# Kernel optimization log

Measured on AMD Instinct MI355X. Metric: run time of the kernel, lower is better.

The kernel has to match this reference:

```python
import jax, jax.numpy as jnp
import numpy as np

B, T, C, H = 2, 2048, 1024, 16
HD = C // H
MAX_WAVELENGTH = 10000.0


def apply_rope(x, positions):
    # x: [B, H, T, HD], positions: [T]
    fraction = 2.0 * jnp.arange(HD // 2, dtype=jnp.float32) / HD
    timescale = MAX_WAVELENGTH ** fraction  # [HD//2]
    sinusoid = positions[:, None] / timescale[None, :]  # [T, HD//2]
    sin = jnp.sin(sinusoid)
    cos = jnp.cos(sinusoid)
    first, second = jnp.split(x, 2, axis=-1)
    out = jnp.concatenate(
        [first * cos - second * sin, second * cos + first * sin], axis=-1
    )
    return out.astype(x.dtype)


def setup_inputs() -> dict:
    key = jax.random.key(0)
    k1, k2, k3 = jax.random.split(key, 3)
    x = jax.random.normal(k1, (B, T, C), dtype=jnp.float32)
    w_attn = jax.random.normal(k2, (C, 3 * C), dtype=jnp.float32) * 0.02
    b_attn = jnp.zeros((3 * C,), dtype=jnp.float32)
    w_proj = jax.random.normal(k3, (C, C), dtype=jnp.float32) * 0.02
    b_proj = jnp.zeros((C,), dtype=jnp.float32)
    return {"x": x, "w_attn": w_attn, "b_attn": b_attn,
            "w_proj": w_proj, "b_proj": b_proj}


def reference(x, w_attn, b_attn, w_proj, b_proj):
    b, t, c = x.shape
    qkv = x @ w_attn + b_attn  # [B, T, 3C]
    q, k, v = jnp.split(qkv, 3, axis=-1)
    q = q.reshape(b, t, H, HD).transpose(0, 2, 1, 3)  # [B, H, T, HD]
    k = k.reshape(b, t, H, HD).transpose(0, 2, 1, 3)
    v = v.reshape(b, t, H, HD).transpose(0, 2, 1, 3)
    positions = jnp.arange(t, dtype=x.dtype)
    q = apply_rope(q, positions)
    k = apply_rope(k, positions)
    att = jnp.einsum('bhqd,bhkd->bhqk', q, k) * (1.0 / jnp.sqrt(HD))
    causal = jnp.tril(jnp.ones((t, t), dtype=bool))
    att = jnp.where(causal, att, jnp.finfo(att.dtype).min)
    att = jax.nn.softmax(att, axis=-1)
    y = jnp.einsum('bhqk,bhkd->bhqd', att, v)
    y = y.transpose(0, 2, 1, 3).reshape(b, t, c)
    return y @ w_proj + b_proj
```

## Files before the change

kernel.cpp:

```cpp
#include <hip/hip_runtime.h>
#include <hip/hip_bf16.h>


typedef __attribute__((ext_vector_type(8))) short short8;
typedef __attribute__((ext_vector_type(4))) float floatx4;

__device__ __forceinline__ unsigned short f2bf(float f) {
    union { float f; unsigned int u; } v; v.f = f;
    unsigned int r = v.u + 0x7FFFu + ((v.u >> 16) & 1u);
    return (unsigned short)(r >> 16);
}

__device__ __forceinline__ unsigned int pk2bf(float a, float b) {
    union { float f; unsigned int u; } ua, ub;
    ua.f = a; ub.f = b;
    return __builtin_amdgcn_perm(ub.u + 0x8000u, ua.u + 0x8000u, 0x07060302u);
}

__device__ __forceinline__ void gld16(const void* g, void* l) {
    __builtin_amdgcn_global_load_lds(
        (const __attribute__((address_space(1))) unsigned int*)g,
        (__attribute__((address_space(3))) unsigned int*)l, 16, 0, 0);
}

__device__ __forceinline__ void transpose_body(
    const float* __restrict__ in, unsigned short* __restrict__ out,
    int R, int NC, int bx, int by, int tid,
    unsigned short (*tile)[65]) {
    int r0 = by * 64, c0 = bx * 64;
    int col = tid & 63, rr = tid >> 6;
#pragma unroll
    for (int i = 0; i < 16; i++) {
        int row = rr + i * 4;
        tile[row][col] = f2bf(in[(size_t)(r0 + row) * NC + c0 + col]);
    }
    __syncthreads();
#pragma unroll
    for (int i = 0; i < 16; i++) {
        int orow = rr + i * 4;
        out[(size_t)(c0 + orow) * R + r0 + col] = tile[col][orow];
    }
}

__global__ __launch_bounds__(256) void prep(
    const float* __restrict__ x,
    const float* __restrict__ w_attn,
    const float* __restrict__ w_proj,
    unsigned short* __restrict__ x_bf,
    unsigned short* __restrict__ wTa,
    unsigned short* __restrict__ wTp,
    float2* __restrict__ tab) {
    __shared__ unsigned short tile[64][65];
    int bid = blockIdx.x;
    int tid = threadIdx.x;
    if (bid < 4096) {
        int i = bid * 256 + tid;
        float4 v = ((const float4*)x)[i];
        ushort4 o;
        o.x = f2bf(v.x); o.y = f2bf(v.y); o.z = f2bf(v.z); o.w = f2bf(v.w);
        ((ushort4*)x_bf)[i] = o;
    } else if (bid < 4864) {
        int t = bid - 4096;
        transpose_body(w_attn, wTa, 1024, 3072, t % 48, t / 48, tid, tile);
    } else if (bid < 5120) {
        int t = bid - 4864;
        transpose_body(w_proj, wTp, 1024, 1024, t & 15, t >> 4, tid, tile);
    } else {
        int i = (bid - 5120) * 256 + tid;
        int t = i >> 5, d = i & 31;
        float inv_ts = exp2f(-0.41524101186092036f * (float)d);
        float ang = (float)t * inv_ts;
        tab[i] = make_float2(sinf(ang), cosf(ang));
    }
}

__global__ __launch_bounds__(256) void gemm_qkv(
    const unsigned short* __restrict__ A,
    const unsigned short* __restrict__ BT,
    const float* __restrict__ bias,
    const float2* __restrict__ tab,
    unsigned short* __restrict__ qT,
    unsigned short* __restrict__ kT,
    unsigned short* __restrict__ vT) {
    __shared__ __align__(16) unsigned short smem[16384];
    unsigned short* as = smem;
    unsigned short* bs = smem + 8192;
    int tid = threadIdx.x;
    int lane = tid & 63;
    int w = tid >> 6;
    int wx = w & 1, wy = w >> 1;
    int l16 = lane & 15, quad = lane >> 4;
    int m0 = blockIdx.y * 128;
    int n0 = blockIdx.x * 128;
    int x = l16 & 7;
    int lr = lane >> 3;
    int gc = (lane & 7) ^ lr;

    floatx4 acc[4][4];
#pragma unroll
    for (int mi = 0; mi < 4; mi++)
#pragma unroll
        for (int ni = 0; ni < 4; ni++)
            acc[mi][ni] = (floatx4){0.f, 0.f, 0.f, 0.f};

    for (int k0 = 0; k0 < 1024; k0 += 64) {
        __syncthreads();
#pragma unroll
        for (int i = 0; i < 4; i++) {
            int seg = w * 4 + i;
            int row = seg * 8 + lr;
            gld16(A + (size_t)(m0 + row) * 1024 + k0 + gc * 8, &as[seg * 512]);
            gld16(BT + (size_t)(n0 + row) * 1024 + k0 + gc * 8, &bs[seg * 512]);
        }
        __syncthreads();
#pragma unroll
        for (int kk = 0; kk < 2; kk++) {
            short8 af[4], bf[4];
#pragma unroll
            for (int mi = 0; mi < 4; mi++) {
                int r = wy * 64 + mi * 16 + l16;
                af[mi] = *(const short8*)&as[r * 64 + (((kk << 2) | quad) ^ x) * 8];
            }
#pragma unroll
            for (int ni = 0; ni < 4; ni++) {
                int r = wx * 64 + ni * 16 + l16;
                bf[ni] = *(const short8*)&bs[r * 64 + (((kk << 2) | quad) ^ x) * 8];
            }
#pragma unroll
            for (int mi = 0; mi < 4; mi++)
#pragma unroll
                for (int ni = 0; ni < 4; ni++)
                    acc[mi][ni] = __builtin_amdgcn_mfma_f32_16x16x32_bf16(
                        af[mi], bf[ni], acc[mi][ni], 0, 0, 0);
        }
    }

    int region = n0 >> 10;
    int b = m0 >> 11;
    float b0 = bias[n0 + wx * 64 + l16];
    float b1 = bias[n0 + wx * 64 + 16 + l16];
    float b2 = bias[n0 + wx * 64 + 32 + l16];
    float b3 = bias[n0 + wx * 64 + 48 + l16];

    if (region < 2) {
        unsigned short* qk = region ? kT : qT;
        float scale = region ? 1.0f : 0.125f;
        int h = ((n0 & 1023) + wx * 64) >> 6;
        unsigned short* obase = qk + (size_t)(b * 16 + h) * 2048 * 64;
#pragma unroll
        for (int mi = 0; mi < 4; mi++)
#pragma unroll
            for (int r = 0; r < 4; r++) {
                int t = (m0 & 2047) + wy * 64 + mi * 16 + quad * 4 + r;
                float2 sc0 = tab[t * 32 + l16];
                float2 sc1 = tab[t * 32 + 16 + l16];
                float v1 = acc[mi][0][r] + b0, v2 = acc[mi][2][r] + b2;
                float w1 = acc[mi][1][r] + b1, w2 = acc[mi][3][r] + b3;
                unsigned short* orow = obase + (size_t)t * 64;
                orow[l16]      = f2bf((v1 * sc0.y - v2 * sc0.x) * scale);
                orow[l16 + 32] = f2bf((v2 * sc0.y + v1 * sc0.x) * scale);
                orow[l16 + 16] = f2bf((w1 * sc1.y - w2 * sc1.x) * scale);
                orow[l16 + 48] = f2bf((w2 * sc1.y + w1 * sc1.x) * scale);
            }
    } else {
        __syncthreads();
#pragma unroll
        for (int mi = 0; mi < 4; mi++)
#pragma unroll
            for (int ni = 0; ni < 4; ni++) {
                int d_loc = wx * 64 + ni * 16 + l16;
                int t_base = wy * 64 + mi * 16 + quad * 4;
                float bv = (ni == 0) ? b0 : (ni == 1) ? b1 : (ni == 2) ? b2 : b3;
                uint2 pk;
                pk.x = pk2bf(acc[mi][ni][0] + bv, acc[mi][ni][1] + bv);
                pk.y = pk2bf(acc[mi][ni][2] + bv, acc[mi][ni][3] + bv);
                int e = d_loc * 128 + (t_base ^ ((d_loc & 15) << 3));
                *(uint2*)&smem[e] = pk;
            }
        __syncthreads();
        int d_r = tid >> 1, half = tid & 1;
        int cv = (n0 - 2048) + d_r;
        int hh = cv >> 6, dd = cv & 63;
        int fofs = (d_r & 15) << 3;
        size_t vbase = ((size_t)(b * 16 + hh) * 64 + dd) * 2048 + (m0 & 2047);
#pragma unroll
        for (int c = 0; c < 8; c++) {
            int tc = half * 64 + c * 8;
            short8 val = *(const short8*)&smem[d_r * 128 + (tc ^ fofs)];
            *(short8*)&vT[vbase + tc] = val;
        }
    }
}

__global__ __launch_bounds__(256) void gemm_proj(
    const unsigned short* __restrict__ A,
    const unsigned short* __restrict__ BT,
    const float* __restrict__ bias,
    float* __restrict__ out) {
    __shared__ __align__(16) unsigned short as[128 * 64];
    __shared__ __align__(16) unsigned short bs[64 * 64];
    int lane = threadIdx.x & 63;
    int w = threadIdx.x >> 6;
    int wx = w & 1, wy = w >> 1;
    int l16 = lane & 15, quad = lane >> 4;
    int m0 = blockIdx.y * 128;
    int n0 = blockIdx.x * 64;
    int x = l16 & 7;
    int lr = lane >> 3;
    int gc = (lane & 7) ^ lr;

    floatx4 acc[4][2];
#pragma unroll
    for (int mi = 0; mi < 4; mi++)
#pragma unroll
        for (int ni = 0; ni < 2; ni++)
            acc[mi][ni] = (floatx4){0.f, 0.f, 0.f, 0.f};

    for (int k0 = 0; k0 < 1024; k0 += 64) {
        __syncthreads();
#pragma unroll
        for (int i = 0; i < 6; i++) {
            int seg = w * 6 + i;
            if (seg < 16) {
                int row = seg * 8 + lr;
                gld16(A + (size_t)(m0 + row) * 1024 + k0 + gc * 8, &as[seg * 512]);
            } else {
                int s2 = seg - 16;
                int row = s2 * 8 + lr;
                gld16(BT + (size_t)(n0 + row) * 1024 + k0 + gc * 8, &bs[s2 * 512]);
            }
        }
        __syncthreads();
#pragma unroll
        for (int kk = 0; kk < 2; kk++) {
            short8 af[4], bf[2];
#pragma unroll
            for (int mi = 0; mi < 4; mi++) {
                int r = wy * 64 + mi * 16 + l16;
                af[mi] = *(const short8*)&as[r * 64 + (((kk << 2) | quad) ^ x) * 8];
            }
#pragma unroll
            for (int ni = 0; ni < 2; ni++) {
                int r = wx * 32 + ni * 16 + l16;
                bf[ni] = *(const short8*)&bs[r * 64 + (((kk << 2) | quad) ^ x) * 8];
            }
#pragma unroll
            for (int mi = 0; mi < 4; mi++)
#pragma unroll
                for (int ni = 0; ni < 2; ni++)
                    acc[mi][ni] = __builtin_amdgcn_mfma_f32_16x16x32_bf16(
                        af[mi], bf[ni], acc[mi][ni], 0, 0, 0);
        }
    }

#pragma unroll
    for (int mi = 0; mi < 4; mi++)
#pragma unroll
        for (int ni = 0; ni < 2; ni++) {
            int row = m0 + wy * 64 + mi * 16 + quad * 4;
            int col = n0 + wx * 32 + ni * 16 + l16;
            float bv = bias[col];
#pragma unroll
            for (int r = 0; r < 4; r++)
                out[(size_t)(row + r) * 1024 + col] = acc[mi][ni][r] + bv;
        }
}

__global__ __launch_bounds__(512) void attn4(
    const unsigned short* __restrict__ qT,
    const unsigned short* __restrict__ kT,
    const unsigned short* __restrict__ vT,
    unsigned short* __restrict__ y) {
    __shared__ __align__(16) unsigned short kbuf[2][64 * 64];
    __shared__ __align__(16) unsigned short vbuf[2][64 * 64];
    __shared__ __align__(16) unsigned short pl[8][16 * 88];
    int lane = threadIdx.x & 63;
    int w = threadIdx.x >> 6;
    int l16 = lane & 15, quad = lane >> 4;
    int blk = blockIdx.x;
    int idx = blk >> 5;
    int qb = (idx < 8) ? (15 - idx * 2) : ((idx - 8) * 2);
    int bh = blk & 31;
    int b = bh >> 4, h = bh & 15;
    int q0 = qb * 128 + w * 16;
    int dt = 2 * qb + (w >> 2);
    const unsigned short* qp = qT + (size_t)bh * 2048 * 64;
    const unsigned short* kp = kT + (size_t)bh * 2048 * 64;
    const unsigned short* vp = vT + (size_t)bh * 64 * 2048;
    unsigned short* plw = pl[w];
    int x = l16 & 7;

    short8 qf0 = *(const short8*)(qp + (size_t)(q0 + l16) * 64 + quad * 8);
    short8 qf1 = *(const short8*)(qp + (size_t)(q0 + l16) * 64 + 32 + quad * 8);

    floatx4 acc[4];
#pragma unroll
    for (int ni = 0; ni < 4; ni++) acc[ni] = (floatx4){0.f, 0.f, 0.f, 0.f};
    float l_part = 0.f;

    auto stage = [&](int bi, int j0) {
#pragma unroll
        for (int i = 0; i < 2; i++) {
            int t = w * 2 + i;
            if (t < 8) {
                int r = t * 8 + (lane >> 3);
                int c = (lane & 7) ^ (r & 7);
                gld16(kp + (size_t)(j0 + r) * 64 + c * 8, &kbuf[bi][t * 512]);
            } else {
                int s = t - 8;
                int d = s * 8 + (lane >> 3);
                int c = (lane & 7) ^ (d & 7);
                gld16(vp + (size_t)d * 2048 + j0 + c * 8, &vbuf[bi][s * 512]);
            }
        }
    };

    int L = 2 * qb + 2;
    stage(0, 0);
    for (int it = 0; it < L; it++) {
        int j0 = it * 64;
        int bi = it & 1;
        __syncthreads();
        if (it + 1 < L) stage(bi ^ 1, j0 + 64);
        if (it > dt) continue;
        const unsigned short* kb = kbuf[bi];
        const unsigned short* vb = vbuf[bi];
        bool diag = (it == dt);
        floatx4 s[4];
#pragma unroll
        for (int c = 0; c < 4; c++) {
            int r = c * 16 + l16;
            short8 kf0 = *(const short8*)&kb[r * 64 + ((quad) ^ x) * 8];
            short8 kf1 = *(const short8*)&kb[r * 64 + ((quad | 4) ^ x) * 8];
            floatx4 z = (floatx4){0.f, 0.f, 0.f, 0.f};
            z = __builtin_amdgcn_mfma_f32_16x16x32_bf16(kf0, qf0, z, 0, 0, 0);
            z = __builtin_amdgcn_mfma_f32_16x16x32_bf16(kf1, qf1, z, 0, 0, 0);
            s[c] = z;
        }
        int query = q0 + l16;
#pragma unroll
        for (int c = 0; c < 4; c++) {
            float p[4];
#pragma unroll
            for (int r = 0; r < 4; r++) {
                float e = __expf(s[c][r]);
                if (diag) {
                    int key = j0 + c * 16 + quad * 4 + r;
                    e = (key <= query) ? e : 0.f;
                }
                p[r] = e;
            }
            l_part += (p[0] + p[1]) + (p[2] + p[3]);
            uint2 pk = {pk2bf(p[0], p[1]), pk2bf(p[2], p[3])};
            *(uint2*)&plw[l16 * 88 + c * 16 + quad * 4] = pk;
        }
        short8 pa0 = *(const short8*)&plw[l16 * 88 + quad * 8];
        short8 pa1 = *(const short8*)&plw[l16 * 88 + 32 + quad * 8];
#pragma unroll
        for (int ni = 0; ni < 4; ni++) {
            int d = ni * 16 + l16;
            short8 vf0 = *(const short8*)&vb[d * 64 + ((quad) ^ x) * 8];
            short8 vf1 = *(const short8*)&vb[d * 64 + ((quad | 4) ^ x) * 8];
            acc[ni] = __builtin_amdgcn_mfma_f32_16x16x32_bf16(pa0, vf0, acc[ni], 0, 0, 0);
            acc[ni] = __builtin_amdgcn_mfma_f32_16x16x32_bf16(pa1, vf1, acc[ni], 0, 0, 0);
        }
    }

    float tot = l_part;
    tot += __shfl_xor(tot, 16, 64);
    tot += __shfl_xor(tot, 32, 64);
    float inv[4];
#pragma unroll
    for (int r = 0; r < 4; r++)
        inv[r] = 1.f / __shfl(tot, quad * 4 + r, 16);
#pragma unroll
    for (int ni = 0; ni < 4; ni++)
#pragma unroll
        for (int r = 0; r < 4; r++) {
            int t = q0 + quad * 4 + r;
            y[((size_t)(b * 2048 + t)) * 1024 + h * 64 + ni * 16 + l16] =
                f2bf(acc[ni][r] * inv[r]);
        }
}

extern "C" void kernel_launch(void* const* d_in, const int* in_sizes, int n_in,
                              void* d_out, int out_size, void* d_ws, size_t ws_size,
                              hipStream_t stream) {
    const float* x      = (const float*)d_in[0];
    const float* w_attn = (const float*)d_in[1];
    const float* b_attn = (const float*)d_in[2];
    const float* w_proj = (const float*)d_in[3];
    const float* b_proj = (const float*)d_in[4];
    float* out = (float*)d_out;

    char* ws = (char*)d_ws;
    unsigned short* x_bf = (unsigned short*)ws;
    unsigned short* wTa  = (unsigned short*)(ws + (8ull << 20));
    unsigned short* wTp  = (unsigned short*)(ws + (14ull << 20));
    unsigned short* qTb  = (unsigned short*)(ws + (16ull << 20));
    unsigned short* kTb  = (unsigned short*)(ws + (24ull << 20));
    unsigned short* vTb  = (unsigned short*)(ws + (32ull << 20));
    float2*         tab  = (float2*)(ws + (40ull << 20));
    unsigned short* y_bf = x_bf;

    prep<<<5376, 256, 0, stream>>>(x, w_attn, w_proj, x_bf, wTa, wTp, tab);
    gemm_qkv<<<dim3(24, 32), 256, 0, stream>>>(x_bf, wTa, b_attn, tab,
                                               qTb, kTb, vTb);
    attn4<<<512, 512, 0, stream>>>(qTb, kTb, vTb, y_bf);
    gemm_proj<<<dim3(16, 32), 256, 0, stream>>>(y_bf, wTp, b_proj, out);
}
```

Baseline: 186.8 us.

## Double-buffer LDS tiles in QKV and proj GEMMs and coalesce Q/K stores

Both GEMM kernels now use two LDS buffers, so the async global-to-LDS load of the next K tile is issued before computing on the current tile, removing one barrier per iteration and overlapping loads with MFMA work. The QKV epilogue for Q/K regions first writes the rope-rotated bf16 results into padded LDS rows and then stores full 16-byte vectors per row instead of scattered 2-byte stores. This doubles LDS usage per block (64KB for qkv), which may reduce occupancy.

```diff
diff --git a/kernel.cpp b/kernel.cpp
--- a/kernel.cpp
+++ b/kernel.cpp
@@ -82,9 +82,7 @@
     unsigned short* __restrict__ qT,
     unsigned short* __restrict__ kT,
     unsigned short* __restrict__ vT) {
-    __shared__ __align__(16) unsigned short smem[16384];
-    unsigned short* as = smem;
-    unsigned short* bs = smem + 8192;
+    __shared__ __align__(16) unsigned short smem[32768];
     int tid = threadIdx.x;
     int lane = tid & 63;
     int w = tid >> 6;
@@ -103,8 +101,9 @@
         for (int ni = 0; ni < 4; ni++)
             acc[mi][ni] = (floatx4){0.f, 0.f, 0.f, 0.f};
 
-    for (int k0 = 0; k0 < 1024; k0 += 64) {
-        __syncthreads();
+    auto stage = [&](int bsel, int k0) {
+        unsigned short* as = smem + bsel * 16384;
+        unsigned short* bs = as + 8192;
 #pragma unroll
         for (int i = 0; i < 4; i++) {
             int seg = w * 4 + i;
@@ -112,7 +111,11 @@
             gld16(A + (size_t)(m0 + row) * 1024 + k0 + gc * 8, &as[seg * 512]);
             gld16(BT + (size_t)(n0 + row) * 1024 + k0 + gc * 8, &bs[seg * 512]);
         }
-        __syncthreads();
+    };
+
+    auto compute = [&](int bsel) {
+        const unsigned short* as = smem + bsel * 16384;
+        const unsigned short* bs = as + 8192;
 #pragma unroll
         for (int kk = 0; kk < 2; kk++) {
             short8 af[4], bf[4];
@@ -133,7 +136,19 @@
                     acc[mi][ni] = __builtin_amdgcn_mfma_f32_16x16x32_bf16(
                         af[mi], bf[ni], acc[mi][ni], 0, 0, 0);
         }
-    }
+    };
+
+    stage(0, 0);
+    __syncthreads();
+    int cur = 0;
+    for (int k0 = 0; k0 < 960; k0 += 64) {
+        stage(cur ^ 1, k0 + 64);
+        compute(cur);
+        __syncthreads();
+        cur ^= 1;
+    }
+    compute(cur);
+    __syncthreads();
 
     int region = n0 >> 10;
     int b = m0 >> 11;
@@ -145,25 +160,37 @@
     if (region < 2) {
         unsigned short* qk = region ? kT : qT;
         float scale = region ? 1.0f : 0.125f;
-        int h = ((n0 & 1023) + wx * 64) >> 6;
-        unsigned short* obase = qk + (size_t)(b * 16 + h) * 2048 * 64;
+        unsigned short* lq = smem;
 #pragma unroll
         for (int mi = 0; mi < 4; mi++)
 #pragma unroll
             for (int r = 0; r < 4; r++) {
-                int t = (m0 & 2047) + wy * 64 + mi * 16 + quad * 4 + r;
+                int tl = wy * 64 + mi * 16 + quad * 4 + r;
+                int t = (m0 & 2047) + tl;
                 float2 sc0 = tab[t * 32 + l16];
                 float2 sc1 = tab[t * 32 + 16 + l16];
                 float v1 = acc[mi][0][r] + b0, v2 = acc[mi][2][r] + b2;
                 float w1 = acc[mi][1][r] + b1, w2 = acc[mi][3][r] + b3;
-                unsigned short* orow = obase + (size_t)t * 64;
+                unsigned short* orow = lq + tl * 136 + wx * 64;
                 orow[l16]      = f2bf((v1 * sc0.y - v2 * sc0.x) * scale);
                 orow[l16 + 32] = f2bf((v2 * sc0.y + v1 * sc0.x) * scale);
                 orow[l16 + 16] = f2bf((w1 * sc1.y - w2 * sc1.x) * scale);
                 orow[l16 + 48] = f2bf((w2 * sc1.y + w1 * sc1.x) * scale);
             }
+        __syncthreads();
+        int c8 = tid & 7;
+        int hl = (tid >> 3) & 1;
+        int tl0 = tid >> 4;
+        int h = ((n0 & 1023) >> 6) + hl;
+        unsigned short* ob = qk + (size_t)(b * 16 + h) * 2048 * 64;
+#pragma unroll
+        for (int p = 0; p < 8; p++) {
+            int tl = p * 16 + tl0;
+            int t = (m0 & 2047) + tl;
+            short8 val = *(const short8*)&lq[tl * 136 + hl * 64 + c8 * 8];
+            *(short8*)&ob[(size_t)t * 64 + c8 * 8] = val;
+        }
     } else {
-        __syncthreads();
 #pragma unroll
         for (int mi = 0; mi < 4; mi++)
 #pragma unroll
@@ -197,8 +224,7 @@
     const unsigned short* __restrict__ BT,
     const float* __restrict__ bias,
     float* __restrict__ out) {
-    __shared__ __align__(16) unsigned short as[128 * 64];
-    __shared__ __align__(16) unsigned short bs[64 * 64];
+    __shared__ __align__(16) unsigned short smem[24576];
     int lane = threadIdx.x & 63;
     int w = threadIdx.x >> 6;
     int wx = w & 1, wy = w >> 1;
@@ -216,8 +242,9 @@
         for (int ni = 0; ni < 2; ni++)
             acc[mi][ni] = (floatx4){0.f, 0.f, 0.f, 0.f};
 
-    for (int k0 = 0; k0 < 1024; k0 += 64) {
-        __syncthreads();
+    auto stage = [&](int bsel, int k0) {
+        unsigned short* as = smem + bsel * 12288;
+        unsigned short* bs = as + 8192;
 #pragma unroll
         for (int i = 0; i < 6; i++) {
             int seg = w * 6 + i;
@@ -230,7 +257,11 @@
                 gld16(BT + (size_t)(n0 + row) * 1024 + k0 + gc * 8, &bs[s2 * 512]);
             }
         }
-        __syncthreads();
+    };
+
+    auto compute = [&](int bsel) {
+        const unsigned short* as = smem + bsel * 12288;
+        const unsigned short* bs = as + 8192;
 #pragma unroll
         for (int kk = 0; kk < 2; kk++) {
             short8 af[4], bf[2];
@@ -251,7 +282,18 @@
                     acc[mi][ni] = __builtin_amdgcn_mfma_f32_16x16x32_bf16(
                         af[mi], bf[ni], acc[mi][ni], 0, 0, 0);
         }
-    }
+    };
+
+    stage(0, 0);
+    __syncthreads();
+    int cur = 0;
+    for (int k0 = 0; k0 < 960; k0 += 64) {
+        stage(cur ^ 1, k0 + 64);
+        compute(cur);
+        __syncthreads();
+        cur ^= 1;
+    }
+    compute(cur);
 
 #pragma unroll
     for (int mi = 0; mi < 4; mi++)
```

New measurement: 182.0 us. -2.6%, faster.
